# Kernel tuning notes

Measured on AMD Instinct MI355X. Metric: run time of the kernel, lower is better.

Reference implementation:

```python
import jax, jax.numpy as jnp
import numpy as np

NUM_SAMPLES = 1024


def _cdist(a, b):
    # a, b: (n, 3) -> (n, n) pairwise euclidean distances (torch.cdist p=2)
    d2 = jnp.sum((a[:, None, :] - b[None, :, :]) ** 2, axis=-1)
    return jnp.sqrt(jnp.maximum(d2, 0.0))


def _greedy_match_cost(cost):
    # Greedy sequential matching: repeatedly take the global argmin over
    # still-unmatched rows/cols, accumulate its cost, eliminate row+col.
    n = cost.shape[0]

    def step(carry, _):
        row_mask, col_mask, loss = carry
        valid = row_mask[:, None] & col_mask[None, :]
        masked = jnp.where(valid, cost, jnp.inf)
        idx = jnp.argmin(masked)  # row-major first-min == torch's min(dim=1)+argmin tiebreak
        r = idx // n
        c = idx % n
        loss = loss + cost[r, c]
        return (row_mask.at[r].set(False), col_mask.at[c].set(False), loss), None

    init = (jnp.ones((n,), dtype=bool), jnp.ones((n,), dtype=bool), jnp.float32(0.0))
    (_, _, loss), _ = jax.lax.scan(step, init, None, length=n)
    return loss / n


def setup_inputs() -> dict:
    key = jax.random.key(0)
    k1, k2, k3 = jax.random.split(key, 3)
    B, N, n = 8, 4096, NUM_SAMPLES
    S1 = jax.random.normal(k1, (B, N, 3), dtype=jnp.float32)
    S2 = jax.random.normal(k2, (B, N, 3), dtype=jnp.float32)
    # torch.randperm(N)[:n] per batch element: without-replacement sampling
    perm_keys = jax.random.split(k3, B)
    indices = jax.vmap(lambda k: jax.random.permutation(k, N)[:n])(perm_keys).astype(jnp.int32)
    return {"S1": S1, "S2": S2, "indices": indices}


def reference(S1, S2, indices):
    # sample the same indices from both sets, per batch (matches original loop)
    s1 = jnp.take_along_axis(S1, indices[:, :, None], axis=1)  # (B, n, 3)
    s2 = jnp.take_along_axis(S2, indices[:, :, None], axis=1)  # (B, n, 3)
    cost = jax.vmap(_cdist)(s1, s2)  # (B, n, n)
    losses = jax.vmap(_greedy_match_cost)(cost)  # (B,)
    return jnp.mean(losses)
```

## Files before the change

### kernel.cpp

```cpp
#include <hip/hip_runtime.h>
#include <stdint.h>

#define BATCH 8
#define NPTS 4096
#define NS 1024
#define KD 6

typedef unsigned long long u64;
typedef unsigned int u32;
typedef unsigned short u16;
typedef unsigned char u8;

#define DEADV (~0ull)
#define QNANB 0x7FC00000u

__device__ __forceinline__ float pdist3(float ax, float ay, float az,
                                        float bx, float by, float bz) {
    float dx = ax - bx, dy = ay - by, dz = az - bz;
    float d2 = __fmaf_rn(dz, dz, __fmaf_rn(dy, dy, dx * dx));
    return __fsqrt_rn(d2);
}

__device__ __forceinline__ u64 packv(float d, u32 row, u32 col) {
    return ((u64)__float_as_uint(d) << 20) | ((u64)row << 10) | (u64)col;
}

__device__ __forceinline__ u64 u64min2(u64 a, u64 b) { return a < b ? a : b; }
__device__ __forceinline__ u64 u64max2(u64 a, u64 b) { return a > b ? a : b; }

__device__ __forceinline__ u64 tree16(const u64* p) {
    u64 a0 = u64min2(p[0], p[1]),   a1 = u64min2(p[2], p[3]);
    u64 a2 = u64min2(p[4], p[5]),   a3 = u64min2(p[6], p[7]);
    u64 a4 = u64min2(p[8], p[9]),   a5 = u64min2(p[10], p[11]);
    u64 a6 = u64min2(p[12], p[13]), a7 = u64min2(p[14], p[15]);
    u64 b0 = u64min2(a0, a1), b1 = u64min2(a2, a3);
    u64 b2 = u64min2(a4, a5), b3 = u64min2(a6, a7);
    return u64min2(u64min2(b0, b1), u64min2(b2, b3));
}

template<int CTRL>
__device__ __forceinline__ u64 dpp_min_step(u64 m) {
    u32 lo = (u32)m, hi = (u32)(m >> 32);
    u32 olo = (u32)__builtin_amdgcn_update_dpp(-1, (int)lo, CTRL, 0xF, 0xF, false);
    u32 ohi = (u32)__builtin_amdgcn_update_dpp(-1, (int)hi, CTRL, 0xF, 0xF, false);
    u64 o = ((u64)ohi << 32) | olo;
    return o < m ? o : m;
}

__device__ __forceinline__ u64 wave_min_u64(u64 m) {
    m = dpp_min_step<0x111>(m);
    m = dpp_min_step<0x112>(m);
    m = dpp_min_step<0x114>(m);
    m = dpp_min_step<0x118>(m);
    m = dpp_min_step<0x142>(m);
    m = dpp_min_step<0x143>(m);
    u32 lo = (u32)__builtin_amdgcn_readlane((int)(u32)m, 63);
    u32 hi = (u32)__builtin_amdgcn_readlane((int)(u32)(m >> 32), 63);
    return ((u64)hi << 32) | lo;
}

__global__ void gather_k(const float* __restrict__ S1, const float* __restrict__ S2,
                         const int* __restrict__ idx,
                         float4* __restrict__ s1g, float4* __restrict__ s2g,
                         int* __restrict__ cnt) {
    int t = blockIdx.x * blockDim.x + threadIdx.x;
    if (t == 0) *cnt = 0;
    if (t >= BATCH * NS) return;
    int b = t >> 10;
    int j = idx[t];
    const float* p1 = S1 + ((size_t)b * NPTS + j) * 3;
    const float* p2 = S2 + ((size_t)b * NPTS + j) * 3;
    s1g[t] = make_float4(p1[0], p1[1], p1[2], 0.f);
    s2g[t] = make_float4(p2[0], p2[1], p2[2], 0.f);
}

__global__ void lists_k(const float4* __restrict__ s1g, const float4* __restrict__ s2g,
                        u64* __restrict__ rlist_g, u64* __restrict__ clist_g) {
    int gg = blockIdx.x * 4 + (threadIdx.x >> 6);
    int lane = threadIdx.x & 63;
    int side = (gg >= BATCH * NS) ? 1 : 0;
    int g = gg - side * (BATCH * NS);
    int b = g >> 10;
    u32 rc = (u32)(g & 1023);
    float4 a = side ? s2g[g] : s1g[g];
    const float4* other = (side ? s1g : s2g) + (size_t)b * NS;
    u64 cand[16];
    #pragma unroll
    for (int k = 0; k < 16; ++k) {
        int o = lane + (k << 6);
        float4 q = other[o];
        float d = pdist3(a.x, a.y, a.z, q.x, q.y, q.z);
        cand[k] = side ? packv(d, (u32)o, rc) : packv(d, rc, (u32)o);
    }
    u64* out = (side ? clist_g : rlist_g) + (size_t)g * KD;
    for (int i = 0; i < KD; ++i) {
        u64 m1 = wave_min_u64(tree16(cand));
        if (lane == 0) out[i] = m1;
        #pragma unroll
        for (int k = 0; k < 16; ++k) cand[k] = (cand[k] == m1) ? DEADV : cand[k];
    }
}

__global__ void __launch_bounds__(1024, 1)
resolve_k(const float4* __restrict__ s1g, const float4* __restrict__ s2g,
          const u64* __restrict__ rlist_gl, const u64* __restrict__ clist_gl,
          float* __restrict__ loss_ws, int* __restrict__ cnt,
          float* __restrict__ out) {
    __shared__ u64 rlist[NS * KD];
    __shared__ u64 clist[NS * KD];
    __shared__ u64 rmin[NS];
    __shared__ u64 cmin[NS];
    __shared__ float4 s1p[NS];
    __shared__ float4 s2p[NS];
    __shared__ u8 rptrs[NS], cptrs[NS];
    __shared__ u16 qrow[NS], qcol[NS];
    __shared__ u16 lrows[NS], lcols[NS];
    __shared__ float lred[1024];
    __shared__ int qrn, qcn, matched, nlr, nlc, stale_n;
    int b = blockIdx.x;
    int tid = threadIdx.x;
    int lane = tid & 63, wv = tid >> 6;

    {
        const float4* rs = (const float4*)(rlist_gl + (size_t)b * NS * KD);
        const float4* cs = (const float4*)(clist_gl + (size_t)b * NS * KD);
        float4* rd = (float4*)rlist;
        float4* cd = (float4*)clist;
        for (int i = tid; i < NS * KD / 2; i += 1024) { rd[i] = rs[i]; cd[i] = cs[i]; }
    }
    s1p[tid] = s1g[(size_t)b * NS + tid];
    s2p[tid] = s2g[(size_t)b * NS + tid];
    rptrs[tid] = 1; cptrs[tid] = 1;
    lrows[tid] = (u16)tid; lcols[tid] = (u16)tid;
    if (tid == 0) { matched = 0; stale_n = NS; }
    __syncthreads();
    rmin[tid] = rlist[tid * KD];
    cmin[tid] = clist[tid * KD];
    float loss = 0.f;
    __syncthreads();

    for (int round = 0; round < NS; ++round) {
        u64 myk = rmin[tid];
        u32 c = (u32)myk & 1023u;
        bool mut = (myk != DEADV) && (cmin[c] == myk);
        __syncthreads();
        if (mut) {
            loss += __uint_as_float((u32)(myk >> 20));
            rmin[tid] = DEADV;
            cmin[c] = DEADV;
            s1p[tid].x = __uint_as_float(QNANB);
            s2p[c].x   = __uint_as_float(QNANB);
        }
        u64 bal = __ballot((int)mut);
        if (lane == 0 && bal) atomicAdd(&matched, (int)__popcll(bal));
        if (tid == 0) { qrn = 0; qcn = 0; nlr = 0; nlc = 0; }
        __syncthreads();
        int m = matched;
        if (m >= NS) break;
        int live = NS - m;
        int stale = stale_n;
        bool rebuild = (stale * 4 > live * 5 + 64);
        u64 rk = rmin[tid];
        if (rk != DEADV) {
            float pr = s2p[(u32)rk & 1023u].x;
            if (pr != pr) {
                u32 p = rptrs[tid];
                bool found = false;
                while (p < KD) {
                    u64 e = rlist[tid * KD + p];
                    ++p;
                    if (e != DEADV) {
                        float q = s2p[(u32)e & 1023u].x;
                        if (q == q) { rmin[tid] = e; found = true; break; }
                    }
                }
                rptrs[tid] = (u8)p;
                if (!found) { int s = atomicAdd(&qrn, 1); qrow[s] = (u16)tid; }
            }
        }
        u64 ck = cmin[tid];
        if (ck != DEADV) {
            float pr = s1p[((u32)ck >> 10) & 1023u].x;
            if (pr != pr) {
                u32 p = cptrs[tid];
                bool found = false;
                while (p < KD) {
                    u64 e = clist[tid * KD + p];
                    ++p;
                    if (e != DEADV) {
                        float q = s1p[((u32)e >> 10) & 1023u].x;
                        if (q == q) { cmin[tid] = e; found = true; break; }
                    }
                }
                cptrs[tid] = (u8)p;
                if (!found) { int s = atomicAdd(&qcn, 1); qcol[s] = (u16)tid; }
            }
        }
        if (rebuild) {
            float cx = s2p[tid].x;
            bool calive = (cx == cx);
            u64 cb = __ballot((int)calive);
            int crank = (int)__popcll(cb & ((1ull << lane) - 1ull));
            int cbase = 0;
            if (lane == 0) cbase = atomicAdd(&nlc, (int)__popcll(cb));
            cbase = __shfl(cbase, 0, 64);
            if (calive) lcols[cbase + crank] = (u16)tid;

            float rx = s1p[tid].x;
            bool ralive = (rx == rx);
            u64 rb = __ballot((int)ralive);
            int rrank = (int)__popcll(rb & ((1ull << lane) - 1ull));
            int rbase = 0;
            if (lane == 0) rbase = atomicAdd(&nlr, (int)__popcll(rb));
            rbase = __shfl(rbase, 0, 64);
            if (ralive) lrows[rbase + rrank] = (u16)tid;
        }
        __syncthreads();
        int nr = qrn, nc = qcn;
        int scan_n = rebuild ? live : stale;
        if (rebuild && tid == 0) stale_n = live;
        for (int qi = wv; qi < nr; qi += 16) {
            u32 r = qrow[qi];
            float4 a = s1p[r];
            u64 m1 = DEADV, m2 = DEADV;
            for (int i = lane; i < scan_n; i += 64) {
                int cc = lcols[i];
                float4 q = s2p[cc];
                float d = pdist3(a.x, a.y, a.z, q.x, q.y, q.z);
                u64 p = packv(d, r, (u32)cc);
                u64 mx = u64max2(p, m1);
                m1 = u64min2(m1, p);
                m2 = u64min2(m2, mx);
            }
            u64 M1 = wave_min_u64(m1);
            u64 c2 = (m1 == M1) ? m2 : m1;
            u64 M2 = wave_min_u64(c2);
            if (lane == 0) {
                rmin[r] = M1;
                rlist[r * KD + KD - 1] = M2;
                rptrs[r] = KD - 1;
            }
        }
        for (int qi = wv; qi < nc; qi += 16) {
            u32 cc = qcol[qi];
            float4 a = s2p[cc];
            u64 m1 = DEADV, m2 = DEADV;
            for (int i = lane; i < scan_n; i += 64) {
                int r = lrows[i];
                float4 q = s1p[r];
                float d = pdist3(q.x, q.y, q.z, a.x, a.y, a.z);
                u64 p = packv(d, (u32)r, cc);
                u64 mx = u64max2(p, m1);
                m1 = u64min2(m1, p);
                m2 = u64min2(m2, mx);
            }
            u64 M1 = wave_min_u64(m1);
            u64 c2 = (m1 == M1) ? m2 : m1;
            u64 M2 = wave_min_u64(c2);
            if (lane == 0) {
                cmin[cc] = M1;
                clist[cc * KD + KD - 1] = M2;
                cptrs[cc] = KD - 1;
            }
        }
        __syncthreads();
    }

    lred[tid] = loss;
    __syncthreads();
    #pragma unroll
    for (int s = 512; s > 0; s >>= 1) {
        if (tid < s) lred[tid] += lred[tid + s];
        __syncthreads();
    }
    if (tid == 0) {
        atomicExch(&loss_ws[b], lred[0] * (1.0f / NS));
        __threadfence();
        int old = atomicAdd(cnt, 1);
        if (old == BATCH - 1) {
            __threadfence();
            float s = 0.f;
            for (int i = 0; i < BATCH; ++i) s += atomicAdd(&loss_ws[i], 0.0f);
            out[0] = s * (1.0f / BATCH);
        }
    }
}

extern "C" void kernel_launch(void* const* d_in, const int* in_sizes, int n_in,
                              void* d_out, int out_size, void* d_ws, size_t ws_size,
                              hipStream_t stream) {
    const float* S1 = (const float*)d_in[0];
    const float* S2 = (const float*)d_in[1];
    const int* idx  = (const int*)d_in[2];
    char* ws = (char*)d_ws;
    size_t o = 0;
    float4* s1g    = (float4*)(ws + o); o += (size_t)BATCH * NS * 16;
    float4* s2g    = (float4*)(ws + o); o += (size_t)BATCH * NS * 16;
    u64* rlist_g   = (u64*)(ws + o);    o += (size_t)BATCH * NS * KD * 8;
    u64* clist_g   = (u64*)(ws + o);    o += (size_t)BATCH * NS * KD * 8;
    float* loss_ws = (float*)(ws + o);  o += (size_t)BATCH * 4;
    int* cnt       = (int*)(ws + o);

    gather_k<<<(BATCH * NS + 255) / 256, 256, 0, stream>>>(S1, S2, idx, s1g, s2g, cnt);
    lists_k<<<2 * BATCH * NS / 4, 256, 0, stream>>>(s1g, s2g, rlist_g, clist_g);
    resolve_k<<<BATCH, 1024, 0, stream>>>(s1g, s2g, rlist_g, clist_g, loss_ws, cnt,
                                          (float*)d_out);
}
```

Before: 198.8 us.

## Use SoA shared coordinates, merge row/col rescans, stage points in LDS

Result: slower. 210.5 us (+5.9%).

```diff
diff --git a/kernel.cpp b/kernel.cpp
--- a/kernel.cpp
+++ b/kernel.cpp
@@ -76,19 +76,22 @@
 
 __global__ void lists_k(const float4* __restrict__ s1g, const float4* __restrict__ s2g,
                         u64* __restrict__ rlist_g, u64* __restrict__ clist_g) {
+    __shared__ float4 pts[NS];
     int gg = blockIdx.x * 4 + (threadIdx.x >> 6);
     int lane = threadIdx.x & 63;
     int side = (gg >= BATCH * NS) ? 1 : 0;
     int g = gg - side * (BATCH * NS);
     int b = g >> 10;
     u32 rc = (u32)(g & 1023);
+    const float4* other = (side ? s1g : s2g) + (size_t)b * NS;
+    for (int i = threadIdx.x; i < NS; i += 256) pts[i] = other[i];
     float4 a = side ? s2g[g] : s1g[g];
-    const float4* other = (side ? s1g : s2g) + (size_t)b * NS;
+    __syncthreads();
     u64 cand[16];
     #pragma unroll
     for (int k = 0; k < 16; ++k) {
         int o = lane + (k << 6);
-        float4 q = other[o];
+        float4 q = pts[o];
         float d = pdist3(a.x, a.y, a.z, q.x, q.y, q.z);
         cand[k] = side ? packv(d, (u32)o, rc) : packv(d, rc, (u32)o);
     }
@@ -110,8 +113,8 @@
     __shared__ u64 clist[NS * KD];
     __shared__ u64 rmin[NS];
     __shared__ u64 cmin[NS];
-    __shared__ float4 s1p[NS];
-    __shared__ float4 s2p[NS];
+    __shared__ float s1xs[NS], s1ys[NS], s1zs[NS];
+    __shared__ float s2xs[NS], s2ys[NS], s2zs[NS];
     __shared__ u8 rptrs[NS], cptrs[NS];
     __shared__ u16 qrow[NS], qcol[NS];
     __shared__ u16 lrows[NS], lcols[NS];
@@ -128,8 +131,12 @@
         float4* cd = (float4*)clist;
         for (int i = tid; i < NS * KD / 2; i += 1024) { rd[i] = rs[i]; cd[i] = cs[i]; }
     }
-    s1p[tid] = s1g[(size_t)b * NS + tid];
-    s2p[tid] = s2g[(size_t)b * NS + tid];
+    {
+        float4 v1 = s1g[(size_t)b * NS + tid];
+        s1xs[tid] = v1.x; s1ys[tid] = v1.y; s1zs[tid] = v1.z;
+        float4 v2 = s2g[(size_t)b * NS + tid];
+        s2xs[tid] = v2.x; s2ys[tid] = v2.y; s2zs[tid] = v2.z;
+    }
     rptrs[tid] = 1; cptrs[tid] = 1;
     lrows[tid] = (u16)tid; lcols[tid] = (u16)tid;
     if (tid == 0) { matched = 0; stale_n = NS; }
@@ -148,8 +155,8 @@
             loss += __uint_as_float((u32)(myk >> 20));
             rmin[tid] = DEADV;
             cmin[c] = DEADV;
-            s1p[tid].x = __uint_as_float(QNANB);
-            s2p[c].x   = __uint_as_float(QNANB);
+            s1xs[tid] = __uint_as_float(QNANB);
+            s2xs[c]   = __uint_as_float(QNANB);
         }
         u64 bal = __ballot((int)mut);
         if (lane == 0 && bal) atomicAdd(&matched, (int)__popcll(bal));
@@ -162,7 +169,7 @@
         bool rebuild = (stale * 4 > live * 5 + 64);
         u64 rk = rmin[tid];
         if (rk != DEADV) {
-            float pr = s2p[(u32)rk & 1023u].x;
+            float pr = s2xs[(u32)rk & 1023u];
             if (pr != pr) {
                 u32 p = rptrs[tid];
                 bool found = false;
@@ -170,7 +177,7 @@
                     u64 e = rlist[tid * KD + p];
                     ++p;
                     if (e != DEADV) {
-                        float q = s2p[(u32)e & 1023u].x;
+                        float q = s2xs[(u32)e & 1023u];
                         if (q == q) { rmin[tid] = e; found = true; break; }
                     }
                 }
@@ -180,7 +187,7 @@
         }
         u64 ck = cmin[tid];
         if (ck != DEADV) {
-            float pr = s1p[((u32)ck >> 10) & 1023u].x;
+            float pr = s1xs[((u32)ck >> 10) & 1023u];
             if (pr != pr) {
                 u32 p = cptrs[tid];
                 bool found = false;
@@ -188,7 +195,7 @@
                     u64 e = clist[tid * KD + p];
                     ++p;
                     if (e != DEADV) {
-                        float q = s1p[((u32)e >> 10) & 1023u].x;
+                        float q = s1xs[((u32)e >> 10) & 1023u];
                         if (q == q) { cmin[tid] = e; found = true; break; }
                     }
                 }
@@ -197,7 +204,7 @@
             }
         }
         if (rebuild) {
-            float cx = s2p[tid].x;
+            float cx = s2xs[tid];
             bool calive = (cx == cx);
             u64 cb = __ballot((int)calive);
             int crank = (int)__popcll(cb & ((1ull << lane) - 1ull));
@@ -206,7 +213,7 @@
             cbase = __shfl(cbase, 0, 64);
             if (calive) lcols[cbase + crank] = (u16)tid;
 
-            float rx = s1p[tid].x;
+            float rx = s1xs[tid];
             bool ralive = (rx == rx);
             u64 rb = __ballot((int)ralive);
             int rrank = (int)__popcll(rb & ((1ull << lane) - 1ull));
@@ -219,48 +226,70 @@
         int nr = qrn, nc = qcn;
         int scan_n = rebuild ? live : stale;
         if (rebuild && tid == 0) stale_n = live;
-        for (int qi = wv; qi < nr; qi += 16) {
-            u32 r = qrow[qi];
-            float4 a = s1p[r];
-            u64 m1 = DEADV, m2 = DEADV;
-            for (int i = lane; i < scan_n; i += 64) {
-                int cc = lcols[i];
-                float4 q = s2p[cc];
-                float d = pdist3(a.x, a.y, a.z, q.x, q.y, q.z);
-                u64 p = packv(d, r, (u32)cc);
-                u64 mx = u64max2(p, m1);
-                m1 = u64min2(m1, p);
-                m2 = u64min2(m2, mx);
-            }
-            u64 M1 = wave_min_u64(m1);
-            u64 c2 = (m1 == M1) ? m2 : m1;
-            u64 M2 = wave_min_u64(c2);
-            if (lane == 0) {
-                rmin[r] = M1;
-                rlist[r * KD + KD - 1] = M2;
-                rptrs[r] = KD - 1;
-            }
-        }
-        for (int qi = wv; qi < nc; qi += 16) {
-            u32 cc = qcol[qi];
-            float4 a = s2p[cc];
-            u64 m1 = DEADV, m2 = DEADV;
-            for (int i = lane; i < scan_n; i += 64) {
-                int r = lrows[i];
-                float4 q = s1p[r];
-                float d = pdist3(q.x, q.y, q.z, a.x, a.y, a.z);
-                u64 p = packv(d, (u32)r, cc);
-                u64 mx = u64max2(p, m1);
-                m1 = u64min2(m1, p);
-                m2 = u64min2(m2, mx);
-            }
-            u64 M1 = wave_min_u64(m1);
-            u64 c2 = (m1 == M1) ? m2 : m1;
-            u64 M2 = wave_min_u64(c2);
-            if (lane == 0) {
-                cmin[cc] = M1;
-                clist[cc * KD + KD - 1] = M2;
-                cptrs[cc] = KD - 1;
+        int tot = nr + nc;
+        for (int qi = wv; qi < tot; qi += 16) {
+            if (qi < nr) {
+                u32 r = qrow[qi];
+                float ax = s1xs[r], ay = s1ys[r], az = s1zs[r];
+                u64 a1 = DEADV, a2 = DEADV, b1 = DEADV, b2 = DEADV;
+                int i = lane;
+                for (; i + 64 < scan_n; i += 128) {
+                    int c0 = lcols[i], c1 = lcols[i + 64];
+                    float d0 = pdist3(ax, ay, az, s2xs[c0], s2ys[c0], s2zs[c0]);
+                    float d1 = pdist3(ax, ay, az, s2xs[c1], s2ys[c1], s2zs[c1]);
+                    u64 p0 = packv(d0, r, (u32)c0);
+                    u64 p1 = packv(d1, r, (u32)c1);
+                    u64 x0 = u64max2(p0, a1); a1 = u64min2(a1, p0); a2 = u64min2(a2, x0);
+                    u64 x1 = u64max2(p1, b1); b1 = u64min2(b1, p1); b2 = u64min2(b2, x1);
+                }
+                if (i < scan_n) {
+                    int c0 = lcols[i];
+                    float d0 = pdist3(ax, ay, az, s2xs[c0], s2ys[c0], s2zs[c0]);
+                    u64 p0 = packv(d0, r, (u32)c0);
+                    u64 x0 = u64max2(p0, a1); a1 = u64min2(a1, p0); a2 = u64min2(a2, x0);
+                }
+                u64 hi = u64max2(a1, b1);
+                u64 m1 = u64min2(a1, b1);
+                u64 m2 = u64min2(hi, u64min2(a2, b2));
+                u64 M1 = wave_min_u64(m1);
+                u64 c2 = (m1 == M1) ? m2 : m1;
+                u64 M2 = wave_min_u64(c2);
+                if (lane == 0) {
+                    rmin[r] = M1;
+                    rlist[r * KD + KD - 1] = M2;
+                    rptrs[r] = KD - 1;
+                }
+            } else {
+                u32 cc = qcol[qi - nr];
+                float ax = s2xs[cc], ay = s2ys[cc], az = s2zs[cc];
+                u64 a1 = DEADV, a2 = DEADV, b1 = DEADV, b2 = DEADV;
+                int i = lane;
+                for (; i + 64 < scan_n; i += 128) {
+                    int r0 = lrows[i], r1 = lrows[i + 64];
+                    float d0 = pdist3(s1xs[r0], s1ys[r0], s1zs[r0], ax, ay, az);
+                    float d1 = pdist3(s1xs[r1], s1ys[r1], s1zs[r1], ax, ay, az);
+                    u64 p0 = packv(d0, (u32)r0, cc);
+                    u64 p1 = packv(d1, (u32)r1, cc);
+                    u64 x0 = u64max2(p0, a1); a1 = u64min2(a1, p0); a2 = u64min2(a2, x0);
+                    u64 x1 = u64max2(p1, b1); b1 = u64min2(b1, p1); b2 = u64min2(b2, x1);
+                }
+                if (i < scan_n) {
+                    int r0 = lrows[i];
+                    float d0 = pdist3(s1xs[r0], s1ys[r0], s1zs[r0], ax, ay, az);
+                    u64 p0 = packv(d0, (u32)r0, cc);
+                    u64 x0 = u64max2(p0, a1); a1 = u64min2(a1, p0); a2 = u64min2(a2, x0);
+                }
+                u64 hi = u64max2(a1, b1);
+                u64 m1 = u64min2(a1, b1);
+                u64 m2 = u64min2(hi, u64min2(a2, b2));
+                u64 M1 = wave_min_u64(m1);
+                u64 c2 = (m1 == M1) ? m2 : m1;
+                u64 M2 = wave_min_u64(c2);
+                if (lane == 0) {
+                    cmin[cc] = M1;
+                    clist[cc * KD + KD - 1] = M2;
+                    cptrs[cc] = KD - 1;
+                }
             }
         }
         __syncthreads();
```
